# Kernel optimization log

Measured on AMD Instinct MI355X. Metric: run time of the kernel, lower is better.

## Reference

```python
import jax, jax.numpy as jnp
import numpy as np

DEPTH = 3
N = 32768          # total nodes
G = 256            # num graphs
P = N // G         # nodes per graph (last node is the virtual node)
E = 524288         # edges
IN, H, H2 = 8, 64, 128


def _lin(key, out_d, in_d):
    w = jax.random.normal(key, (out_d, in_d), dtype=jnp.float32) * (1.0 / np.sqrt(in_d))
    b = jnp.zeros((out_d,), dtype=jnp.float32)
    return w, b


def setup_inputs() -> dict:
    key = jax.random.key(0)
    ks = jax.random.split(key, 10)
    x = jax.random.normal(ks[0], (N, IN), dtype=jnp.float32)
    edge_index = jax.random.randint(ks[1], (2, E), 0, N, dtype=jnp.int32).astype(jnp.int64)
    batch = (jnp.arange(N, dtype=jnp.int64) // P)
    W1, b1 = _lin(ks[2], H, IN)
    W2, b2 = _lin(ks[3], H, H)
    W3, b3 = _lin(ks[4], H, H)
    W4, b4 = _lin(ks[5], H, 2 * H)
    W5, b5 = _lin(ks[6], H, H * H)
    Wd1, bd1 = _lin(ks[7], H2, H)
    Wd2, bd2 = _lin(ks[8], 1, H2)
    return {"x": x, "edge_index": edge_index, "batch": batch, "num_graphs": G,
            "W1": W1, "b1": b1, "W2": W2, "b2": b2, "W3": W3, "b3": b3,
            "W4": W4, "b4": b4, "W5": W5, "b5": b5,
            "Wd1": Wd1, "bd1": bd1, "Wd2": Wd2, "bd2": bd2}


def reference(x, edge_index, batch, num_graphs,
              W1, b1, W2, b2, W3, b3, W4, b4, W5, b5, Wd1, bd1, Wd2, bd2):
    # initial embed: linear -> relu -> L2 normalize
    h = jax.nn.relu(x @ W1.T + b1)
    h = h / jnp.linalg.norm(h, axis=-1, keepdims=True)
    src, dst = edge_index[0], edge_index[1]
    for _ in range(DEPTH):
        # sum-aggregate neighbor messages (PyG add aggregation: gather src, scatter-add to dst)
        m = jax.ops.segment_sum(h[src], dst, num_segments=N)
        cat = jnp.concatenate([m @ W3.T + b3, h @ W2.T + b2], axis=-1)  # [N, 2H]
        h = jax.nn.relu(cat @ W4.T + b4)
        h = h / jnp.linalg.norm(h, axis=-1, keepdims=True)
    # per-graph: outer product of each non-virtual node embedding with the
    # last (virtual) node embedding. Graphs are equal-sized -> vectorize by reshape.
    hg = h.reshape(num_graphs, P, H)
    others = hg[:, :-1, :]          # [G, P-1, H]
    last = hg[:, -1, :]             # [G, H]
    outer = jnp.einsum('gpi,gj->gpij', others, last)        # [G, P-1, H, H]
    outer = outer.reshape(num_graphs * (P - 1), H * H)       # flatten(start_dim=1), row-major i*H+j
    y = outer @ W5.T + b5
    y = jax.nn.relu(y @ Wd1.T + bd1)
    y = y @ Wd2.T + bd2              # [G*(P-1), 1] Q-values
    return y
```

## Files before the change

### kernel.cpp

```cpp
#include <hip/hip_runtime.h>
#include <hip/hip_bf16.h>

#define NN 32768
#define EE 524288
#define GG 256
#define PP 128

__global__ void k_init(const float* __restrict__ x, const float* __restrict__ W1,
                       const float* __restrict__ b1,
                       const float* __restrict__ W2, const float* __restrict__ b2,
                       const float* __restrict__ W3, const float* __restrict__ b3,
                       const float* __restrict__ W4, const float* __restrict__ b4,
                       const float* __restrict__ Wd1,
                       float* __restrict__ h0, float* __restrict__ h1,
                       float* __restrict__ Wc, float* __restrict__ Wd1t,
                       int* __restrict__ deg, int* __restrict__ csr) {
    __shared__ float tile[128 * 65];
    int b = blockIdx.x, t = threadIdx.x;
    if (b >= 8192) {
        if (b == 8224) {
            for (int idx = t; idx < 8192; idx += 256) {
                int q = idx >> 6, o = idx & 63;
                tile[q*65 + o] = Wd1[idx];
            }
            __syncthreads();
            for (int idx = t; idx < 8192; idx += 256) {
                int o = idx >> 7, q = idx & 127;
                Wd1t[idx] = tile[q*65 + o];
            }
        } else if (b == 8225) {
            if (t < 64)       h0[(long)NN*64 + t] = 0.f;
            else if (t < 128) h1[(long)NN*64 + (t-64)] = 0.f;
        } else {
            int idx = (b - 8192) * 256 + t;
            int kk = idx >> 6, o = idx & 63;
            float a = 0.f;
            if (kk < 64) {
                for (int j = 0; j < 64; ++j) a += W4[o*128 + j] * W3[j*64 + kk];
            } else {
                int k2 = kk - 64;
                for (int j = 0; j < 64; ++j) a += W4[o*128 + 64 + j] * W2[j*64 + k2];
            }
            Wc[kk*64 + o] = a;
            if (idx < 64) {
                float c = b4[idx];
                for (int j = 0; j < 64; ++j)
                    c += W4[idx*128 + j]*b3[j] + W4[idx*128 + 64 + j]*b2[j];
                Wc[8192 + idx] = c;
            }
        }
        return;
    }
    if (b < 128) deg[b * 256 + t] = 0;
    if (t < 64)
        ((int4*)csr)[b*64 + t] = make_int4(NN, NN, NN, NN);
    int node = (b * 256 + t) >> 6;
    int lane = t & 63;
    float acc = b1[lane];
    #pragma unroll
    for (int j = 0; j < 8; ++j)
        acc += x[node*8 + j] * W1[lane*8 + j];
    acc = fmaxf(acc, 0.f);
    float ss = acc * acc;
    #pragma unroll
    for (int m = 1; m < 64; m <<= 1) ss += __shfl_xor(ss, m, 64);
    h0[node*64 + lane] = acc / sqrtf(ss);
}

__global__ void k_fill(const int* __restrict__ src, const int* __restrict__ dst,
                       int* __restrict__ deg, int* __restrict__ csr) {
    int i = blockIdx.x * blockDim.x + threadIdx.x;
    int4 s4 = ((const int4*)src)[i];
    int4 d4 = ((const int4*)dst)[i];
    csr[(d4.x << 6) + atomicAdd(&deg[d4.x], 1)] = s4.x;
    csr[(d4.y << 6) + atomicAdd(&deg[d4.y], 1)] = s4.y;
    csr[(d4.z << 6) + atomicAdd(&deg[d4.z], 1)] = s4.z;
    csr[(d4.w << 6) + atomicAdd(&deg[d4.w], 1)] = s4.w;
}

__global__ void __launch_bounds__(256) k_layer(
        const float* __restrict__ Wc, const float* __restrict__ hcur,
        const int* __restrict__ deg, const int* __restrict__ csr,
        float* __restrict__ hnext) {
    __shared__ float Wl[8192];
    __shared__ float Xl[64 * 132];
    int t = threadIdx.x;
    int nbase = blockIdx.x * 64;

    for (int i = t * 4; i < 8192; i += 1024)
        *(float4*)&Wl[i] = *(const float4*)&Wc[i];
    for (int idx = t; idx < 1024; idx += 256) {
        int n = idx >> 4, c = (idx & 15) * 4;
        *(float4*)&Xl[n*132 + 64 + c] = *(const float4*)&hcur[(long)(nbase+n)*64 + c];
    }

    int w = t >> 6, lane = t & 63;
    int fg4 = (lane & 15) * 4, es = lane >> 4;
    int nb = nbase + w * 16;
    int dv = deg[nb + (lane & 15)];
    const int4* base4 = (const int4*)csr + (long)nb * 16;
    int4 iA = base4[es];
    int4 iB = base4[4 + es];
    for (int ni = 0; ni < 16; ++ni) {
        int4 cA = iA, cB = iB;
        if (ni < 15) {
            iA = base4[(ni+1)*16 + es];
            iB = base4[(ni+1)*16 + 4 + es];
        }
        float4 a0 = *(const float4*)&hcur[(long)cA.x*64 + fg4];
        float4 a1 = *(const float4*)&hcur[(long)cA.y*64 + fg4];
        float4 a2 = *(const float4*)&hcur[(long)cA.z*64 + fg4];
        float4 a3 = *(const float4*)&hcur[(long)cA.w*64 + fg4];
        float4 b0 = *(const float4*)&hcur[(long)cB.x*64 + fg4];
        float4 b1 = *(const float4*)&hcur[(long)cB.y*64 + fg4];
        float4 b2 = *(const float4*)&hcur[(long)cB.z*64 + fg4];
        float4 b3 = *(const float4*)&hcur[(long)cB.w*64 + fg4];
        float4 acc;
        acc.x = ((a0.x + a1.x) + (a2.x + a3.x)) + ((b0.x + b1.x) + (b2.x + b3.x));
        acc.y = ((a0.y + a1.y) + (a2.y + a3.y)) + ((b0.y + b1.y) + (b2.y + b3.y));
        acc.z = ((a0.z + a1.z) + (a2.z + a3.z)) + ((b0.z + b1.z) + (b2.z + b3.z));
        acc.w = ((a0.w + a1.w) + (a2.w + a3.w)) + ((b0.w + b1.w) + (b2.w + b3.w));
        int dg = __shfl(dv, ni, 64);
        if (dg > 32) {
            int de4 = (dg + 3) >> 2;
            for (int q = es + 8; q < de4; q += 4) {
                int4 cx = base4[ni*16 + q];
                float4 v0 = *(const float4*)&hcur[(long)cx.x*64 + fg4];
                float4 v1 = *(const float4*)&hcur[(long)cx.y*64 + fg4];
                float4 v2 = *(const float4*)&hcur[(long)cx.z*64 + fg4];
                float4 v3 = *(const float4*)&hcur[(long)cx.w*64 + fg4];
                acc.x += (v0.x + v1.x) + (v2.x + v3.x);
                acc.y += (v0.y + v1.y) + (v2.y + v3.y);
                acc.z += (v0.z + v1.z) + (v2.z + v3.z);
                acc.w += (v0.w + v1.w) + (v2.w + v3.w);
            }
        }
        acc.x += __shfl_xor(acc.x, 16, 64); acc.y += __shfl_xor(acc.y, 16, 64);
        acc.z += __shfl_xor(acc.z, 16, 64); acc.w += __shfl_xor(acc.w, 16, 64);
        acc.x += __shfl_xor(acc.x, 32, 64); acc.y += __shfl_xor(acc.y, 32, 64);
        acc.z += __shfl_xor(acc.z, 32, 64); acc.w += __shfl_xor(acc.w, 32, 64);
        if (es == 0) *(float4*)&Xl[(w*16 + ni)*132 + fg4] = acc;
    }
    __syncthreads();

    int tc = t & 15, tr = t >> 4;
    int o0 = tc * 4, n0 = tr * 4;
    float4 c4 = *(const float4*)&Wc[8192 + o0];
    float acc[4][4] = {};
    #pragma unroll 2
    for (int kk = 0; kk < 128; kk += 4) {
        float4 w0 = *(float4*)&Wl[(kk+0)*64 + o0];
        float4 w1 = *(float4*)&Wl[(kk+1)*64 + o0];
        float4 w2 = *(float4*)&Wl[(kk+2)*64 + o0];
        float4 w3 = *(float4*)&Wl[(kk+3)*64 + o0];
        #pragma unroll
        for (int jn = 0; jn < 4; ++jn) {
            float4 xv = *(float4*)&Xl[(n0+jn)*132 + kk];
            acc[jn][0] += xv.x*w0.x + xv.y*w1.x + xv.z*w2.x + xv.w*w3.x;
            acc[jn][1] += xv.x*w0.y + xv.y*w1.y + xv.z*w2.y + xv.w*w3.y;
            acc[jn][2] += xv.x*w0.z + xv.y*w1.z + xv.z*w2.z + xv.w*w3.z;
            acc[jn][3] += xv.x*w0.w + xv.y*w1.w + xv.z*w2.w + xv.w*w3.w;
        }
    }

    #pragma unroll
    for (int jn = 0; jn < 4; ++jn) {
        float v0 = fmaxf(acc[jn][0] + c4.x, 0.f);
        float v1 = fmaxf(acc[jn][1] + c4.y, 0.f);
        float v2 = fmaxf(acc[jn][2] + c4.z, 0.f);
        float v3 = fmaxf(acc[jn][3] + c4.w, 0.f);
        float ss = v0*v0 + v1*v1 + v2*v2 + v3*v3;
        ss += __shfl_xor(ss, 1, 64);
        ss += __shfl_xor(ss, 2, 64);
        ss += __shfl_xor(ss, 4, 64);
        ss += __shfl_xor(ss, 8, 64);
        float r = 1.0f / sqrtf(ss);
        float4 outv = make_float4(v0*r, v1*r, v2*r, v3*r);
        *(float4*)&hnext[(long)(nbase + n0 + jn)*64 + o0] = outv;
    }
}

__global__ void __launch_bounds__(256) k_tmat(
        const float* __restrict__ h, const float* __restrict__ W5,
        float* __restrict__ Tt) {
    __shared__ float lastL[256 * 65];
    __shared__ float wL[64 * 16];
    __shared__ float tr[16 * 257];
    int t = threadIdx.x;
    int rb = blockIdx.x * 16;
    int i = rb >> 6, obase = rb & 63;

    for (int idx4 = t; idx4 < 4096; idx4 += 256) {
        int g = idx4 >> 4, c = (idx4 & 15) * 4;
        *(float4*)&lastL[g*65 + c] =
            *(const float4*)&h[((long)g*128 + 127)*64 + c];
    }
    {
        int rr = t & 15, j0 = (t >> 4) * 4;
        float4 w = *(const float4*)&W5[(long)(obase + rr)*4096 + i*64 + j0];
        wL[(j0+0)*16 + rr] = w.x;
        wL[(j0+1)*16 + rr] = w.y;
        wL[(j0+2)*16 + rr] = w.z;
        wL[(j0+3)*16 + rr] = w.w;
    }
    __syncthreads();

    int g = t;
    float acc[16] = {};
    for (int j = 0; j < 64; ++j) {
        float lv = lastL[g*65 + j];
        #pragma unroll
        for (int r4 = 0; r4 < 4; ++r4) {
            float4 wv = *(float4*)&wL[j*16 + r4*4];
            acc[r4*4+0] += wv.x * lv;
            acc[r4*4+1] += wv.y * lv;
            acc[r4*4+2] += wv.z * lv;
            acc[r4*4+3] += wv.w * lv;
        }
    }
    #pragma unroll
    for (int rr = 0; rr < 16; ++rr) tr[rr*257 + g] = acc[rr];
    __syncthreads();
    for (int it = 0; it < 4; ++it) {
        int idx = t + it*256;
        int g2 = idx >> 2, c4 = idx & 3;
        float4 v = make_float4(tr[(c4*4+0)*257 + g2], tr[(c4*4+1)*257 + g2],
                               tr[(c4*4+2)*257 + g2], tr[(c4*4+3)*257 + g2]);
        *(float4*)&Tt[(long)g2*4096 + rb + c4*4] = v;
    }
}

__global__ void __launch_bounds__(256) k_readout(
        const float* __restrict__ h, const float* __restrict__ Tt,
        const float* __restrict__ b5, const float* __restrict__ Wd1t,
        const float* __restrict__ bd1, const float* __restrict__ Wd2,
        const float* __restrict__ bd2, float* __restrict__ out) {
    __shared__ float Tl[4096];
    __shared__ float W1t[8192];
    __shared__ float OY[32 * 68];
    int t = threadIdx.x;
    int g = blockIdx.x;

    for (int i = t * 4; i < 4096; i += 1024)
        *(float4*)&Tl[i] = *(const float4*)&Tt[(long)g*4096 + i];
    for (int i = t * 4; i < 8192; i += 1024)
        *(float4*)&W1t[i] = *(const float4*)&Wd1t[i];

    int tc = t & 15, tr = t >> 4;
    int o0 = tc * 4, p0 = tr * 2;
    int tc2 = t & 31, tr2 = t >> 5;
    int q0 = tc2 * 4, pp0 = tr2 * 4;
    float4 b5_4  = *(const float4*)&b5[o0];
    float4 bd1_4 = *(const float4*)&bd1[q0];
    float4 wd2_4 = *(const float4*)&Wd2[q0];
    float bd2v = bd2[0];

    for (int pt = 0; pt < 4; ++pt) {
        int pbase = pt * 32;
        __syncthreads();
        for (int idx = t; idx < 512; idx += 256) {
            int p = idx >> 4, c = (idx & 15) * 4;
            *(float4*)&OY[p*68 + c] =
                *(const float4*)&h[((long)g*128 + pbase + p)*64 + c];
        }
        __syncthreads();

        float a10[4] = {0.f,0.f,0.f,0.f};
        float a11[4] = {0.f,0.f,0.f,0.f};
        #pragma unroll 4
        for (int i = 0; i < 64; i += 4) {
            float4 w0 = *(float4*)&Tl[(i+0)*64 + o0];
            float4 w1 = *(float4*)&Tl[(i+1)*64 + o0];
            float4 w2 = *(float4*)&Tl[(i+2)*64 + o0];
            float4 w3 = *(float4*)&Tl[(i+3)*64 + o0];
            float4 x0 = *(float4*)&OY[(p0+0)*68 + i];
            float4 x1 = *(float4*)&OY[(p0+1)*68 + i];
            a10[0] += x0.x*w0.x + x0.y*w1.x + x0.z*w2.x + x0.w*w3.x;
            a10[1] += x0.x*w0.y + x0.y*w1.y + x0.z*w2.y + x0.w*w3.y;
            a10[2] += x0.x*w0.z + x0.y*w1.z + x0.z*w2.z + x0.w*w3.z;
            a10[3] += x0.x*w0.w + x0.y*w1.w + x0.z*w2.w + x0.w*w3.w;
            a11[0] += x1.x*w0.x + x1.y*w1.x + x1.z*w2.x + x1.w*w3.x;
            a11[1] += x1.x*w0.y + x1.y*w1.y + x1.z*w2.y + x1.w*w3.y;
            a11[2] += x1.x*w0.z + x1.y*w1.z + x1.z*w2.z + x1.w*w3.z;
            a11[3] += x1.x*w0.w + x1.y*w1.w + x1.z*w2.w + x1.w*w3.w;
        }
        __syncthreads();

        float4 y0 = make_float4(a10[0]+b5_4.x, a10[1]+b5_4.y, a10[2]+b5_4.z, a10[3]+b5_4.w);
        float4 y1 = make_float4(a11[0]+b5_4.x, a11[1]+b5_4.y, a11[2]+b5_4.z, a11[3]+b5_4.w);
        *(float4*)&OY[(p0+0)*68 + o0] = y0;
        *(float4*)&OY[(p0+1)*68 + o0] = y1;
        __syncthreads();

        float a2[4][4] = {};
        #pragma unroll 4
        for (int o = 0; o < 64; o += 4) {
            float4 w0 = *(float4*)&W1t[(o+0)*128 + q0];
            float4 w1 = *(float4*)&W1t[(o+1)*128 + q0];
            float4 w2 = *(float4*)&W1t[(o+2)*128 + q0];
            float4 w3 = *(float4*)&W1t[(o+3)*128 + q0];
            #pragma unroll
            for (int jp = 0; jp < 4; ++jp) {
                float4 yv = *(float4*)&OY[(pp0+jp)*68 + o];
                a2[jp][0] += yv.x*w0.x + yv.y*w1.x + yv.z*w2.x + yv.w*w3.x;
                a2[jp][1] += yv.x*w0.y + yv.y*w1.y + yv.z*w2.y + yv.w*w3.y;
                a2[jp][2] += yv.x*w0.z + yv.y*w1.z + yv.z*w2.z + yv.w*w3.z;
                a2[jp][3] += yv.x*w0.w + yv.y*w1.w + yv.z*w2.w + yv.w*w3.w;
            }
        }

        #pragma unroll
        for (int jp = 0; jp < 4; ++jp) {
            float s = wd2_4.x * fmaxf(a2[jp][0] + bd1_4.x, 0.f)
                    + wd2_4.y * fmaxf(a2[jp][1] + bd1_4.y, 0.f)
                    + wd2_4.z * fmaxf(a2[jp][2] + bd1_4.z, 0.f)
                    + wd2_4.w * fmaxf(a2[jp][3] + bd1_4.w, 0.f);
            s += __shfl_xor(s, 1, 64);
            s += __shfl_xor(s, 2, 64);
            s += __shfl_xor(s, 4, 64);
            s += __shfl_xor(s, 8, 64);
            s += __shfl_xor(s, 16, 64);
            if (tc2 == 0) {
                int p = pbase + pp0 + jp;
                if (p < 127) out[g*127 + p] = s + bd2v;
            }
        }
    }
}

extern "C" void kernel_launch(void* const* d_in, const int* in_sizes, int n_in,
                              void* d_out, int out_size, void* d_ws, size_t ws_size,
                              hipStream_t stream) {
    const float* x   = (const float*)d_in[0];
    const int*   ei  = (const int*)d_in[1];
    const float* W1  = (const float*)d_in[4];
    const float* b1  = (const float*)d_in[5];
    const float* W2  = (const float*)d_in[6];
    const float* b2  = (const float*)d_in[7];
    const float* W3  = (const float*)d_in[8];
    const float* b3  = (const float*)d_in[9];
    const float* W4  = (const float*)d_in[10];
    const float* b4  = (const float*)d_in[11];
    const float* W5  = (const float*)d_in[12];
    const float* b5  = (const float*)d_in[13];
    const float* Wd1 = (const float*)d_in[14];
    const float* bd1 = (const float*)d_in[15];
    const float* Wd2 = (const float*)d_in[16];
    const float* bd2 = (const float*)d_in[17];
    float* out = (float*)d_out;

    float* ws  = (float*)d_ws;
    float* h0   = ws;
    float* h1   = ws + 2129984;
    float* Tt   = ws + 4259968;
    float* Wc   = ws + 5308416;
    float* Wd1t = ws + 5316864;
    int*   deg  = (int*)(ws + 5325056);
    int*   csr  = deg + NN;

    const int* src = ei;
    const int* dst = ei + EE;

    k_init<<<8226, 256, 0, stream>>>(x, W1, b1, W2, b2, W3, b3, W4, b4,
                                     Wd1, h0, h1, Wc, Wd1t, deg, csr);
    k_fill<<<512, 256, 0, stream>>>(src, dst, deg, csr);

    float* hc = h0; float* hn = h1;
    for (int l = 0; l < 3; ++l) {
        k_layer<<<NN/64, 256, 0, stream>>>(Wc, hc, deg, csr, hn);
        float* tmp = hc; hc = hn; hn = tmp;
    }

    k_tmat<<<256, 256, 0, stream>>>(hc, W5, Tt);
    k_readout<<<256, 256, 0, stream>>>(hc, Tt, b5, Wd1t, bd1, Wd2, bd2, out);
}
```

Measured before the change: 256.8 us.

## Gather neighbor features from a bf16 copy of node embeddings; split readout across blocks

Each layer and the init kernel now also write a bf16-packed copy of the node embeddings. The neighbor-gather aggregation reads 16-byte bf16 rows (8 features per lane) instead of fp32, halving the bytes fetched per random gather, and widens the edge-slot stride to 8 per wave. The readout kernel is also split so two blocks handle each graph's four point tiles, doubling the grid to 512 blocks. Aggregation precision drops to bf16 inputs with fp32 accumulation, and each layer pays an extra bf16 store.

```diff
diff --git a/kernel.cpp b/kernel.cpp
--- a/kernel.cpp
+++ b/kernel.cpp
@@ -5,6 +5,15 @@
 #define EE 524288
 #define GG 256
 #define PP 128
+
+__device__ inline unsigned int bf16pack2(float a, float b) {
+    unsigned int ua = __float_as_uint(a), ub = __float_as_uint(b);
+    ua += 0x7fffu + ((ua >> 16) & 1u);
+    ub += 0x7fffu + ((ub >> 16) & 1u);
+    return (ua >> 16) | (ub & 0xffff0000u);
+}
+__device__ inline float bflo(unsigned int u) { return __uint_as_float(u << 16); }
+__device__ inline float bfhi(unsigned int u) { return __uint_as_float(u & 0xffff0000u); }
 
 __global__ void k_init(const float* __restrict__ x, const float* __restrict__ W1,
                        const float* __restrict__ b1,
@@ -13,6 +22,7 @@
                        const float* __restrict__ W4, const float* __restrict__ b4,
                        const float* __restrict__ Wd1,
                        float* __restrict__ h0, float* __restrict__ h1,
+                       unsigned int* __restrict__ hb0, unsigned int* __restrict__ hb1,
                        float* __restrict__ Wc, float* __restrict__ Wd1t,
                        int* __restrict__ deg, int* __restrict__ csr) {
     __shared__ float tile[128 * 65];
@@ -31,6 +41,8 @@
         } else if (b == 8225) {
             if (t < 64)       h0[(long)NN*64 + t] = 0.f;
             else if (t < 128) h1[(long)NN*64 + (t-64)] = 0.f;
+            else if (t < 160) hb0[(long)NN*32 + (t-128)] = 0u;
+            else if (t < 192) hb1[(long)NN*32 + (t-160)] = 0u;
         } else {
             int idx = (b - 8192) * 256 + t;
             int kk = idx >> 6, o = idx & 63;
@@ -64,7 +76,11 @@
     float ss = acc * acc;
     #pragma unroll
     for (int m = 1; m < 64; m <<= 1) ss += __shfl_xor(ss, m, 64);
-    h0[node*64 + lane] = acc / sqrtf(ss);
+    float hv = acc / sqrtf(ss);
+    h0[(long)node*64 + lane] = hv;
+    float other = __shfl_xor(hv, 1, 64);
+    if ((lane & 1) == 0)
+        hb0[(long)node*32 + (lane >> 1)] = bf16pack2(hv, other);
 }
 
 __global__ void k_fill(const int* __restrict__ src, const int* __restrict__ dst,
@@ -80,12 +96,22 @@
 
 __global__ void __launch_bounds__(256) k_layer(
         const float* __restrict__ Wc, const float* __restrict__ hcur,
+        const unsigned int* __restrict__ hbcur,
         const int* __restrict__ deg, const int* __restrict__ csr,
-        float* __restrict__ hnext) {
+        float* __restrict__ hnext, unsigned int* __restrict__ hbnext) {
     __shared__ float Wl[8192];
     __shared__ float Xl[64 * 132];
     int t = threadIdx.x;
     int nbase = blockIdx.x * 64;
+
+    int w = t >> 6, lane = t & 63;
+    int fg8 = (lane & 7) * 8;
+    int ug  = (lane & 7) * 4;
+    int es  = lane >> 3;
+    int nb = nbase + w * 16;
+    const int4* base4 = (const int4*)csr + (long)nb * 16;
+    int dv = deg[nb + (lane & 15)];
+    int4 iC = base4[es];
 
     for (int i = t * 4; i < 8192; i += 1024)
         *(float4*)&Wl[i] = *(const float4*)&Wc[i];
@@ -94,52 +120,60 @@
         *(float4*)&Xl[n*132 + 64 + c] = *(const float4*)&hcur[(long)(nbase+n)*64 + c];
     }
 
-    int w = t >> 6, lane = t & 63;
-    int fg4 = (lane & 15) * 4, es = lane >> 4;
-    int nb = nbase + w * 16;
-    int dv = deg[nb + (lane & 15)];
-    const int4* base4 = (const int4*)csr + (long)nb * 16;
-    int4 iA = base4[es];
-    int4 iB = base4[4 + es];
+    uint4 r0 = *(const uint4*)&hbcur[(long)iC.x*32 + ug];
+    uint4 r1 = *(const uint4*)&hbcur[(long)iC.y*32 + ug];
+    uint4 r2 = *(const uint4*)&hbcur[(long)iC.z*32 + ug];
+    uint4 r3 = *(const uint4*)&hbcur[(long)iC.w*32 + ug];
+    int4 iN = base4[16 + es];
     for (int ni = 0; ni < 16; ++ni) {
-        int4 cA = iA, cB = iB;
+        uint4 s0 = r0, s1 = r1, s2 = r2, s3 = r3;
         if (ni < 15) {
-            iA = base4[(ni+1)*16 + es];
-            iB = base4[(ni+1)*16 + 4 + es];
-        }
-        float4 a0 = *(const float4*)&hcur[(long)cA.x*64 + fg4];
-        float4 a1 = *(const float4*)&hcur[(long)cA.y*64 + fg4];
-        float4 a2 = *(const float4*)&hcur[(long)cA.z*64 + fg4];
-        float4 a3 = *(const float4*)&hcur[(long)cA.w*64 + fg4];
-        float4 b0 = *(const float4*)&hcur[(long)cB.x*64 + fg4];
-        float4 b1 = *(const float4*)&hcur[(long)cB.y*64 + fg4];
-        float4 b2 = *(const float4*)&hcur[(long)cB.z*64 + fg4];
-        float4 b3 = *(const float4*)&hcur[(long)cB.w*64 + fg4];
-        float4 acc;
-        acc.x = ((a0.x + a1.x) + (a2.x + a3.x)) + ((b0.x + b1.x) + (b2.x + b3.x));
-        acc.y = ((a0.y + a1.y) + (a2.y + a3.y)) + ((b0.y + b1.y) + (b2.y + b3.y));
-        acc.z = ((a0.z + a1.z) + (a2.z + a3.z)) + ((b0.z + b1.z) + (b2.z + b3.z));
-        acc.w = ((a0.w + a1.w) + (a2.w + a3.w)) + ((b0.w + b1.w) + (b2.w + b3.w));
+            int4 c2 = iN;
+            if (ni < 14) iN = base4[(ni+2)*16 + es];
+            r0 = *(const uint4*)&hbcur[(long)c2.x*32 + ug];
+            r1 = *(const uint4*)&hbcur[(long)c2.y*32 + ug];
+            r2 = *(const uint4*)&hbcur[(long)c2.z*32 + ug];
+            r3 = *(const uint4*)&hbcur[(long)c2.w*32 + ug];
+        }
+        float a0, a1, a2, a3, a4, a5, a6, a7;
+        a0 = bflo(s0.x); a1 = bfhi(s0.x); a2 = bflo(s0.y); a3 = bfhi(s0.y);
+        a4 = bflo(s0.z); a5 = bfhi(s0.z); a6 = bflo(s0.w); a7 = bfhi(s0.w);
+        a0 += bflo(s1.x); a1 += bfhi(s1.x); a2 += bflo(s1.y); a3 += bfhi(s1.y);
+        a4 += bflo(s1.z); a5 += bfhi(s1.z); a6 += bflo(s1.w); a7 += bfhi(s1.w);
+        a0 += bflo(s2.x); a1 += bfhi(s2.x); a2 += bflo(s2.y); a3 += bfhi(s2.y);
+        a4 += bflo(s2.z); a5 += bfhi(s2.z); a6 += bflo(s2.w); a7 += bfhi(s2.w);
+        a0 += bflo(s3.x); a1 += bfhi(s3.x); a2 += bflo(s3.y); a3 += bfhi(s3.y);
+        a4 += bflo(s3.z); a5 += bfhi(s3.z); a6 += bflo(s3.w); a7 += bfhi(s3.w);
         int dg = __shfl(dv, ni, 64);
         if (dg > 32) {
             int de4 = (dg + 3) >> 2;
-            for (int q = es + 8; q < de4; q += 4) {
+            for (int q = es + 8; q < de4; q += 8) {
                 int4 cx = base4[ni*16 + q];
-                float4 v0 = *(const float4*)&hcur[(long)cx.x*64 + fg4];
-                float4 v1 = *(const float4*)&hcur[(long)cx.y*64 + fg4];
-                float4 v2 = *(const float4*)&hcur[(long)cx.z*64 + fg4];
-                float4 v3 = *(const float4*)&hcur[(long)cx.w*64 + fg4];
-                acc.x += (v0.x + v1.x) + (v2.x + v3.x);
-                acc.y += (v0.y + v1.y) + (v2.y + v3.y);
-                acc.z += (v0.z + v1.z) + (v2.z + v3.z);
-                acc.w += (v0.w + v1.w) + (v2.w + v3.w);
-            }
-        }
-        acc.x += __shfl_xor(acc.x, 16, 64); acc.y += __shfl_xor(acc.y, 16, 64);
-        acc.z += __shfl_xor(acc.z, 16, 64); acc.w += __shfl_xor(acc.w, 16, 64);
-        acc.x += __shfl_xor(acc.x, 32, 64); acc.y += __shfl_xor(acc.y, 32, 64);
-        acc.z += __shfl_xor(acc.z, 32, 64); acc.w += __shfl_xor(acc.w, 32, 64);
-        if (es == 0) *(float4*)&Xl[(w*16 + ni)*132 + fg4] = acc;
+                uint4 v0 = *(const uint4*)&hbcur[(long)cx.x*32 + ug];
+                uint4 v1 = *(const uint4*)&hbcur[(long)cx.y*32 + ug];
+                uint4 v2 = *(const uint4*)&hbcur[(long)cx.z*32 + ug];
+                uint4 v3 = *(const uint4*)&hbcur[(long)cx.w*32 + ug];
+                a0 += bflo(v0.x); a1 += bfhi(v0.x); a2 += bflo(v0.y); a3 += bfhi(v0.y);
+                a4 += bflo(v0.z); a5 += bfhi(v0.z); a6 += bflo(v0.w); a7 += bfhi(v0.w);
+                a0 += bflo(v1.x); a1 += bfhi(v1.x); a2 += bflo(v1.y); a3 += bfhi(v1.y);
+                a4 += bflo(v1.z); a5 += bfhi(v1.z); a6 += bflo(v1.w); a7 += bfhi(v1.w);
+                a0 += bflo(v2.x); a1 += bfhi(v2.x); a2 += bflo(v2.y); a3 += bfhi(v2.y);
+                a4 += bflo(v2.z); a5 += bfhi(v2.z); a6 += bflo(v2.w); a7 += bfhi(v2.w);
+                a0 += bflo(v3.x); a1 += bfhi(v3.x); a2 += bflo(v3.y); a3 += bfhi(v3.y);
+                a4 += bflo(v3.z); a5 += bfhi(v3.z); a6 += bflo(v3.w); a7 += bfhi(v3.w);
+            }
+        }
+        #pragma unroll
+        for (int d = 8; d <= 32; d <<= 1) {
+            a0 += __shfl_xor(a0, d, 64); a1 += __shfl_xor(a1, d, 64);
+            a2 += __shfl_xor(a2, d, 64); a3 += __shfl_xor(a3, d, 64);
+            a4 += __shfl_xor(a4, d, 64); a5 += __shfl_xor(a5, d, 64);
+            a6 += __shfl_xor(a6, d, 64); a7 += __shfl_xor(a7, d, 64);
+        }
+        if (es == 0) {
+            *(float4*)&Xl[(w*16 + ni)*132 + fg8]     = make_float4(a0, a1, a2, a3);
+            *(float4*)&Xl[(w*16 + ni)*132 + fg8 + 4] = make_float4(a4, a5, a6, a7);
+        }
     }
     __syncthreads();
 
@@ -176,7 +210,11 @@
         ss += __shfl_xor(ss, 8, 64);
         float r = 1.0f / sqrtf(ss);
         float4 outv = make_float4(v0*r, v1*r, v2*r, v3*r);
-        *(float4*)&hnext[(long)(nbase + n0 + jn)*64 + o0] = outv;
+        long nrow = (long)(nbase + n0 + jn);
+        *(float4*)&hnext[nrow*64 + o0] = outv;
+        unsigned int p0 = bf16pack2(outv.x, outv.y);
+        unsigned int p1 = bf16pack2(outv.z, outv.w);
+        *(uint2*)&hbnext[nrow*32 + (o0 >> 1)] = make_uint2(p0, p1);
     }
 }
 
@@ -239,7 +277,8 @@
     __shared__ float W1t[8192];
     __shared__ float OY[32 * 68];
     int t = threadIdx.x;
-    int g = blockIdx.x;
+    int g = blockIdx.x >> 1;
+    int tile0 = (blockIdx.x & 1) * 2;
 
     for (int i = t * 4; i < 4096; i += 1024)
         *(float4*)&Tl[i] = *(const float4*)&Tt[(long)g*4096 + i];
@@ -255,8 +294,8 @@
     float4 wd2_4 = *(const float4*)&Wd2[q0];
     float bd2v = bd2[0];
 
-    for (int pt = 0; pt < 4; ++pt) {
-        int pbase = pt * 32;
+    for (int pt = 0; pt < 2; ++pt) {
+        int pbase = (tile0 + pt) * 32;
         __syncthreads();
         for (int idx = t; idx < 512; idx += 256) {
             int p = idx >> 4, c = (idx & 15) * 4;
@@ -357,20 +396,24 @@
     float* Wd1t = ws + 5316864;
     int*   deg  = (int*)(ws + 5325056);
     int*   csr  = deg + NN;
+    unsigned int* hb0 = (unsigned int*)(ws + 7454976);
+    unsigned int* hb1 = hb0 + 1048608;
 
     const int* src = ei;
     const int* dst = ei + EE;
 
     k_init<<<8226, 256, 0, stream>>>(x, W1, b1, W2, b2, W3, b3, W4, b4,
-                                     Wd1, h0, h1, Wc, Wd1t, deg, csr);
+                                     Wd1, h0, h1, hb0, hb1, Wc, Wd1t, deg, csr);
     k_fill<<<512, 256, 0, stream>>>(src, dst, deg, csr);
 
     float* hc = h0; float* hn = h1;
+    unsigned int* bc = hb0; unsigned int* bn = hb1;
     for (int l = 0; l < 3; ++l) {
-        k_layer<<<NN/64, 256, 0, stream>>>(Wc, hc, deg, csr, hn);
-        float* tmp = hc; hc = hn; hn = tmp;
+        k_layer<<<NN/64, 256, 0, stream>>>(Wc, hc, bc, deg, csr, hn, bn);
+        float* tf = hc; hc = hn; hn = tf;
+        unsigned int* tb = bc; bc = bn; bn = tb;
     }
 
     k_tmat<<<256, 256, 0, stream>>>(hc, W5, Tt);
-    k_readout<<<256, 256, 0, stream>>>(hc, Tt, b5, Wd1t, bd1, Wd2, bd2, out);
-}
+    k_readout<<<512, 256, 0, stream>>>(hc, Tt, b5, Wd1t, bd1, Wd2, bd2, out);
+}
```

After: 262.1 us. 2.1% more time.
